# Performance work log

Hardware: AMD Instinct MI355X
Metric: run time of the kernel (lower is better)

The kernel has to match this reference:

```python
import jax, jax.numpy as jnp
import numpy as np

B, N, C = 4, 4096, 128

def setup_inputs() -> dict:
    key = jax.random.key(0)
    ks = jax.random.split(key, 7)
    s = 1.0 / np.sqrt(C)
    return {
        "x": jax.random.normal(ks[0], (B, N, C), dtype=jnp.float32),
        "Wq": jax.random.uniform(ks[1], (C, C), jnp.float32, -s, s),
        "bq": jax.random.uniform(ks[2], (C,), jnp.float32, -s, s),
        "Wk": jax.random.uniform(ks[3], (C, C), jnp.float32, -s, s),
        "bk": jax.random.uniform(ks[4], (C,), jnp.float32, -s, s),
        "Wv": jax.random.uniform(ks[5], (C, C), jnp.float32, -s, s),
        "bv": jax.random.uniform(ks[6], (C,), jnp.float32, -s, s),
    }

def reference(x, Wq, bq, Wk, bk, Wv, bv):
    # GELU-activated Q/K/V projections (torch default GELU = exact erf form)
    q = jax.nn.gelu(jnp.einsum("bnc,dc->bnd", x, Wq) + bq, approximate=False)
    k = jax.nn.gelu(jnp.einsum("bnc,dc->bnd", x, Wk) + bk, approximate=False)
    v = jax.nn.gelu(jnp.einsum("bnc,dc->bnd", x, Wv) + bv, approximate=False)
    # Unscaled attention: softmax(Q K^T) V
    scores = jnp.einsum("bnd,bmd->bnm", q, k)  # [B, N, N]
    attn = jax.nn.softmax(scores, axis=-1)
    return jnp.einsum("bnm,bmd->bnd", attn, v)
```

## Files before the change

### kernel.cpp

```cpp
#include <hip/hip_runtime.h>
#include <hip/hip_bf16.h>
#include <math.h>

#define BATCH 4
#define SEQ   4096
#define CDIM  128
#define NROWS (BATCH * SEQ)
#define KVB   32
#define NTILE (SEQ / KVB)
#define KTILE_B 8192
#define VTILE_B 8192
#define STAGE_B (KTILE_B + VTILE_B)
#define LOG2E 1.4426950408889634f

typedef __attribute__((ext_vector_type(4))) float    f32x4;
typedef __attribute__((ext_vector_type(8))) _Float16 half8;
typedef __attribute__((ext_vector_type(4))) short    bf16x4;
typedef __attribute__((ext_vector_type(8))) short    bf16x8;

__device__ __forceinline__ float bf2f(short s) {
  unsigned u = ((unsigned)(unsigned short)s) << 16;
  return __builtin_bit_cast(float, u);
}
__device__ __forceinline__ short f2bf(float f) {
  __hip_bfloat16 h = __float2bfloat16(f);
  return __builtin_bit_cast(short, h);
}
__device__ __forceinline__ float gelu_exact(float v) {
  return 0.5f * v * (1.0f + erff(v * 0.70710678118654752440f));
}
__device__ __forceinline__ float exp2_hw(float x) {
  float r;
  asm("v_exp_f32 %0, %1\n\ts_nop 0" : "=v"(r) : "v"(x));
  return r;
}
__device__ __forceinline__ int kswz_h(int r, int c) {
  int slot  = c >> 3;
  int slotp = (slot & 8) | ((slot ^ r) & 7);
  return r * 128 + slotp * 8 + (c & 7);
}
__device__ __forceinline__ void gl_lds16(const void* g, void* l) {
  __builtin_amdgcn_global_load_lds(
      (const __attribute__((address_space(1))) void*)g,
      (__attribute__((address_space(3))) void*)l, 16, 0, 0);
}

__global__ void wprep_kernel(const float* __restrict__ Wq,
                             const float* __restrict__ Wk,
                             const float* __restrict__ Wv,
                             _Float16* __restrict__ wfrag) {
  int mat = blockIdx.y;
  const float* W = (mat == 0) ? Wq : ((mat == 1) ? Wk : Wv);
  int i = blockIdx.x * 256 + threadIdx.x;
  int d = i >> 7, c = i & 127;
  int nt = d >> 4, qr = d & 15, cc = c >> 5, g = (c >> 3) & 3, j = c & 7;
  wfrag[(size_t)((((mat * 8 + nt) * 4 + cc) * 64) + 16 * g + qr) * 8 + j] =
      (_Float16)W[i];
}

__global__ __launch_bounds__(256) void proj_kernel(
    const float* __restrict__ x, const _Float16* __restrict__ wfrag,
    const float* __restrict__ bq, const float* __restrict__ bk,
    const float* __restrict__ bv,
    _Float16* __restrict__ qfrag, _Float16* __restrict__ kimg,
    short* __restrict__ vimg) {
  __shared__ __align__(16) char pls[16384];
  const int tid = threadIdx.x, wave = tid >> 6, lane = tid & 63;
  const int g = lane >> 4, qr = lane & 15;
  const int row0 = blockIdx.x * 64 + wave * 16;

  half8 xf[4];
#pragma unroll
  for (int c4 = 0; c4 < 4; ++c4) {
    const float* px = x + (size_t)(row0 + qr) * CDIM + 8 * g + 32 * c4;
    f32x4 a = *(const f32x4*)px;
    f32x4 bb = *(const f32x4*)(px + 4);
    half8 hx;
#pragma unroll
    for (int j = 0; j < 4; ++j) { hx[j] = (_Float16)a[j]; hx[4 + j] = (_Float16)bb[j]; }
    xf[c4] = hx;
  }

#pragma unroll
  for (int mat = 0; mat < 3; ++mat) {
    const float* bias = (mat == 0) ? bq : ((mat == 1) ? bk : bv);
    f32x4 acc[8];
#pragma unroll
    for (int nt = 0; nt < 8; ++nt) acc[nt] = (f32x4){0.f, 0.f, 0.f, 0.f};
#pragma unroll
    for (int nt = 0; nt < 8; ++nt)
#pragma unroll
      for (int c4 = 0; c4 < 4; ++c4) {
        half8 wf = *(const half8*)(wfrag +
            ((size_t)(((mat * 8 + nt) * 4 + c4) * 64) + lane) * 8);
        acc[nt] = __builtin_amdgcn_mfma_f32_16x16x32_f16(xf[c4], wf, acc[nt], 0, 0, 0);
      }

    short* ls = (short*)pls;
#pragma unroll
    for (int nt = 0; nt < 8; ++nt) {
      int col = 16 * nt + qr;
      float bi = bias[col];
#pragma unroll
      for (int r = 0; r < 4; ++r) {
        int rl = wave * 16 + 4 * g + r;
        float val = gelu_exact(acc[nt][r] + bi);
        int off;
        short sv;
        if (mat == 0) {
          int lane2 = ((col >> 3) & 3) * 16 + (rl & 15);
          off = ((wave * 4 + (col >> 5)) * 64 + lane2) * 8 + (col & 7);
          sv = __builtin_bit_cast(short, (_Float16)(val * LOG2E));
        } else if (mat == 1) {
          int tl = rl >> 5, rr = rl & 31;
          off = tl * 4096 + kswz_h(rr, col);
          sv = __builtin_bit_cast(short, (_Float16)val);
        } else {
          int tl = rl >> 5, rr = rl & 31;
          int klin = 8 * ((rr >> 2) & 3) + (rr & 3) + 4 * (rr >> 4);
          int slotp = (klin >> 3) ^ ((col >> 1) & 3);
          off = tl * 4096 + col * 32 + slotp * 8 + (klin & 7);
          sv = f2bf(val);
        }
        ls[off] = sv;
      }
    }
    __syncthreads();
    char* gdst = (mat == 0) ? (char*)qfrag + (size_t)blockIdx.x * 16384
               : (mat == 1) ? (char*)kimg + (size_t)blockIdx.x * 16384
                            : (char*)vimg + (size_t)blockIdx.x * 16384;
#pragma unroll
    for (int p = 0; p < 4; ++p)
      ((f32x4*)gdst)[tid + 256 * p] = ((const f32x4*)pls)[tid + 256 * p];
    __syncthreads();
  }
}

template <int NSPLIT>
__global__ __launch_bounds__(256, 2) void attn_kernel(
    const _Float16* __restrict__ qfrag, const char* __restrict__ kimg,
    const char* __restrict__ vimg, short* __restrict__ pacc,
    float* __restrict__ pml) {
  __shared__ __align__(16) char smem[2][STAGE_B];
  constexpr int NT = NTILE / NSPLIT;
  const int tid = threadIdx.x, wave = tid >> 6, lane = tid & 63;
  const int g = lane >> 4, qr = lane & 15;

  const int i = blockIdx.x;
  const int stream = i & (4 * NSPLIT - 1);
  const int b = stream / NSPLIT, sp = stream % NSPLIT;
  const int qg = i / (4 * NSPLIT);

  const int t0 = b * 256 + qg * 8 + wave * 2;
  half8 qf[2][4];
#pragma unroll
  for (int qs = 0; qs < 2; ++qs)
#pragma unroll
    for (int c4 = 0; c4 < 4; ++c4)
      qf[qs][c4] = *(const half8*)(qfrag +
          ((size_t)((t0 + qs) * 4 + c4) * 64 + lane) * 8);

  int koff[4];
#pragma unroll
  for (int c4 = 0; c4 < 4; ++c4) {
    int slot = 4 * c4 + g;
    int slotp = (slot & 8) | ((slot ^ qr) & 7);
    koff[c4] = qr * 256 + slotp * 16;
  }
  const int voff = qr * 64 + ((g ^ ((qr >> 1) & 3)) << 4);

  bf16x8 ones8;
#pragma unroll
  for (int j = 0; j < 8; ++j) ones8[j] = (short)0x3F80;

  const char* kp = kimg + ((size_t)b * NTILE + sp * NT) * KTILE_B + tid * 16;
  const char* vp = vimg + ((size_t)b * NTILE + sp * NT) * VTILE_B + tid * 16;

  auto stage = [&](char* buf) {
    gl_lds16(kp,        buf + tid * 16);
    gl_lds16(kp + 4096, buf + 4096 + tid * 16);
    gl_lds16(vp,        buf + 8192 + tid * 16);
    gl_lds16(vp + 4096, buf + 12288 + tid * 16);
    kp += KTILE_B;
    vp += VTILE_B;
  };

  f32x4 acc[2][8];
#pragma unroll
  for (int qs = 0; qs < 2; ++qs)
#pragma unroll
    for (int dt = 0; dt < 8; ++dt) acc[qs][dt] = (f32x4){0.f, 0.f, 0.f, 0.f};
  f32x4 lacc[2] = {(f32x4){0.f, 0.f, 0.f, 0.f}, (f32x4){0.f, 0.f, 0.f, 0.f}};
  float m[2] = {-INFINITY, -INFINITY};

  stage(smem[0]);

  auto phase = [&](const char* cur, char* other, bool do_stage) {
    asm volatile("s_waitcnt vmcnt(0) lgkmcnt(0)" ::: "memory");
    __builtin_amdgcn_s_barrier();
    if (do_stage) stage(other);

    f32x4 sA[2][2];
#pragma unroll
    for (int s = 0; s < 2; ++s) {
      half8 kf[4];
#pragma unroll
      for (int c4 = 0; c4 < 4; ++c4)
        kf[c4] = *(const half8*)(cur + koff[c4] + s * 4096);
      __builtin_amdgcn_s_setprio(1);
#pragma unroll
      for (int qs = 0; qs < 2; ++qs) {
        f32x4 tac = (f32x4){0.f, 0.f, 0.f, 0.f};
#pragma unroll
        for (int c4 = 0; c4 < 4; ++c4)
          tac = __builtin_amdgcn_mfma_f32_16x16x32_f16(kf[c4], qf[qs][c4], tac, 0, 0, 0);
        sA[qs][s] = tac;
      }
      __builtin_amdgcn_s_setprio(0);
    }

    bf16x8 pf8[2];
#pragma unroll
    for (int qs = 0; qs < 2; ++qs) {
      float tm = fmaxf(
          fmaxf(fmaxf(sA[qs][0][0], sA[qs][0][1]), fmaxf(sA[qs][0][2], sA[qs][0][3])),
          fmaxf(fmaxf(sA[qs][1][0], sA[qs][1][1]), fmaxf(sA[qs][1][2], sA[qs][1][3])));
      tm = fmaxf(tm, __shfl_xor(tm, 16, 64));
      tm = fmaxf(tm, __shfl_xor(tm, 32, 64));
      if (!__all(tm <= m[qs] + 8.0f)) {
        float mn = fmaxf(m[qs], tm);
        float alpha = exp2_hw(m[qs] - mn);
        m[qs] = mn;
        float af[4];
#pragma unroll
        for (int r = 0; r < 4; ++r) af[r] = __shfl(alpha, 4 * g + r, 64);
#pragma unroll
        for (int dt = 0; dt < 8; ++dt)
#pragma unroll
          for (int r = 0; r < 4; ++r) acc[qs][dt][r] *= af[r];
#pragma unroll
        for (int r = 0; r < 4; ++r) lacc[qs][r] *= af[r];
      }
#pragma unroll
      for (int e = 0; e < 8; ++e)
        pf8[qs][e] = f2bf(exp2_hw(sA[qs][e >> 2][e & 3] - m[qs]));
    }

    lacc[0] = __builtin_amdgcn_mfma_f32_16x16x32_bf16(pf8[0], ones8, lacc[0], 0, 0, 0);
    lacc[1] = __builtin_amdgcn_mfma_f32_16x16x32_bf16(pf8[1], ones8, lacc[1], 0, 0, 0);

#pragma unroll
    for (int dt = 0; dt < 8; ++dt) {
      bf16x8 v = *(const bf16x8*)(cur + KTILE_B + voff + dt * 1024);
      __builtin_amdgcn_s_setprio(1);
      acc[0][dt] = __builtin_amdgcn_mfma_f32_16x16x32_bf16(pf8[0], v, acc[0][dt], 0, 0, 0);
      acc[1][dt] = __builtin_amdgcn_mfma_f32_16x16x32_bf16(pf8[1], v, acc[1][dt], 0, 0, 0);
      __builtin_amdgcn_s_setprio(0);
    }
  };

#pragma unroll 1
  for (int it = 0; it < NT / 2; ++it) {
    phase(smem[0], smem[1], true);
    phase(smem[1], smem[0], it != NT / 2 - 1);
  }

  const int lrow0 = qg * 128 + wave * 32;
#pragma unroll
  for (int qs = 0; qs < 2; ++qs) {
#pragma unroll
    for (int dt = 0; dt < 8; ++dt)
#pragma unroll
      for (int r = 0; r < 4; ++r) {
        int grow = b * SEQ + lrow0 + qs * 16 + 4 * g + r;
        pacc[((size_t)sp * NROWS + grow) * CDIM + 16 * dt + qr] =
            f2bf(acc[qs][dt][r]);
      }
    if (g == 0) {
      int grow = b * SEQ + lrow0 + qs * 16 + qr;
      pml[((size_t)sp * NROWS + grow) * 2 + 0] = m[qs];
    }
    if (qr == 0) {
#pragma unroll
      for (int r = 0; r < 4; ++r) {
        int grow = b * SEQ + lrow0 + qs * 16 + 4 * g + r;
        pml[((size_t)sp * NROWS + grow) * 2 + 1] = lacc[qs][r];
      }
    }
  }
}

template <int NSPLIT>
__global__ __launch_bounds__(256) void combine_kernel(
    const short* __restrict__ pacc, const float* __restrict__ pml,
    float* __restrict__ out) {
  int idx = blockIdx.x * 256 + threadIdx.x;
  int row = idx >> 4, c8 = idx & 15;
  float mm[NSPLIT], ll[NSPLIT];
  float M = -INFINITY;
#pragma unroll
  for (int h = 0; h < NSPLIT; ++h) {
    mm[h] = pml[((size_t)h * NROWS + row) * 2 + 0];
    ll[h] = pml[((size_t)h * NROWS + row) * 2 + 1];
    M = fmaxf(M, mm[h]);
  }
  float o[8];
#pragma unroll
  for (int j = 0; j < 8; ++j) o[j] = 0.f;
  float wl = 0.f;
#pragma unroll
  for (int h = 0; h < NSPLIT; ++h) {
    float w = exp2f(mm[h] - M);
    wl += w * ll[h];
    bf16x8 a = ((const bf16x8*)pacc)[((size_t)h * NROWS + row) * 16 + c8];
#pragma unroll
    for (int j = 0; j < 8; ++j) o[j] += w * bf2f(a[j]);
  }
  float inv = 1.0f / wl;
  f32x4 o0 = {o[0] * inv, o[1] * inv, o[2] * inv, o[3] * inv};
  f32x4 o1 = {o[4] * inv, o[5] * inv, o[6] * inv, o[7] * inv};
  ((f32x4*)out)[(size_t)row * 32 + c8 * 2 + 0] = o0;
  ((f32x4*)out)[(size_t)row * 32 + c8 * 2 + 1] = o1;
}

extern "C" void kernel_launch(void* const* d_in, const int* in_sizes, int n_in,
                              void* d_out, int out_size, void* d_ws, size_t ws_size,
                              hipStream_t stream) {
  const float* x  = (const float*)d_in[0];
  const float* Wq = (const float*)d_in[1];
  const float* bq = (const float*)d_in[2];
  const float* Wk = (const float*)d_in[3];
  const float* bk = (const float*)d_in[4];
  const float* Wv = (const float*)d_in[5];
  const float* bv = (const float*)d_in[6];
  float* out = (float*)d_out;

  char* ws = (char*)d_ws;
  _Float16* qfrag = (_Float16*)(ws);
  char*     kimg  = ws + (4u << 20);
  char*     vimg  = ws + (8u << 20);
  _Float16* wfrag = (_Float16*)(ws + (12u << 20));
  char*     tail  = ws + (12u << 20) + (256u << 10);

  const size_t need8 = (12u << 20) + (256u << 10) +
                       (size_t)8 * NROWS * 8 + (size_t)8 * NROWS * CDIM * 2;

  wprep_kernel<<<dim3(64, 3), 256, 0, stream>>>(Wq, Wk, Wv, wfrag);
  proj_kernel<<<NROWS / 64, 256, 0, stream>>>(x, wfrag, bq, bk, bv,
                                              qfrag, (_Float16*)kimg, (short*)vimg);
  if (ws_size >= need8) {
    float* pml  = (float*)tail;
    short* pacc = (short*)(tail + (size_t)8 * NROWS * 8);
    attn_kernel<8><<<1024, 256, 0, stream>>>(qfrag, kimg, vimg, pacc, pml);
    combine_kernel<8><<<NROWS * 16 / 256, 256, 0, stream>>>(pacc, pml, out);
  } else {
    float* pml  = (float*)tail;
    short* pacc = (short*)(tail + (size_t)4 * NROWS * 8);
    attn_kernel<4><<<512, 256, 0, stream>>>(qfrag, kimg, vimg, pacc, pml);
    combine_kernel<4><<<NROWS * 16 / 256, 256, 0, stream>>>(pacc, pml, out);
  }
}
```

Before: 147.1 us.

## Split K and V staging into a triple-buffered K, double-buffered V pipeline

```diff
diff --git a/kernel.cpp b/kernel.cpp
--- a/kernel.cpp
+++ b/kernel.cpp
@@ -10,7 +10,6 @@
 #define NTILE (SEQ / KVB)
 #define KTILE_B 8192
 #define VTILE_B 8192
-#define STAGE_B (KTILE_B + VTILE_B)
 #define LOG2E 1.4426950408889634f
 
 typedef __attribute__((ext_vector_type(4))) float    f32x4;
@@ -136,15 +135,35 @@
   }
 }
 
+#define PHASE(KB, VB, KW, VW, IK, IV, VMK, VMV)                         \
+  do {                                                                  \
+    if (IK) stageK(KW);                                                 \
+    asm volatile("s_waitcnt vmcnt(" VMK ")" ::: "memory");              \
+    __builtin_amdgcn_s_barrier();                                       \
+    if (IV) stageV(VW);                                                 \
+    qk_sm(KB);                                                          \
+    asm volatile("s_waitcnt vmcnt(" VMV ")" ::: "memory");              \
+    __builtin_amdgcn_s_barrier();                                       \
+    pv(VB);                                                             \
+  } while (0)
+
 template <int NSPLIT>
 __global__ __launch_bounds__(256, 2) void attn_kernel(
     const _Float16* __restrict__ qfrag, const char* __restrict__ kimg,
     const char* __restrict__ vimg, short* __restrict__ pacc,
     float* __restrict__ pml) {
-  __shared__ __align__(16) char smem[2][STAGE_B];
+  __shared__ __align__(16) char smem[3 * KTILE_B + 2 * VTILE_B];
   constexpr int NT = NTILE / NSPLIT;
+  static_assert((NT - 4) % 6 == 0, "steady loop needs (NT-4) % 6 == 0");
+  constexpr int NSTEADY = (NT - 4) / 6;
   const int tid = threadIdx.x, wave = tid >> 6, lane = tid & 63;
   const int g = lane >> 4, qr = lane & 15;
+
+  char* const kbuf0 = smem;
+  char* const kbuf1 = smem + KTILE_B;
+  char* const kbuf2 = smem + 2 * KTILE_B;
+  char* const vbuf0 = smem + 3 * KTILE_B;
+  char* const vbuf1 = smem + 3 * KTILE_B + VTILE_B;
 
   const int i = blockIdx.x;
   const int stream = i & (4 * NSPLIT - 1);
@@ -176,12 +195,14 @@
   const char* kp = kimg + ((size_t)b * NTILE + sp * NT) * KTILE_B + tid * 16;
   const char* vp = vimg + ((size_t)b * NTILE + sp * NT) * VTILE_B + tid * 16;
 
-  auto stage = [&](char* buf) {
+  auto stageK = [&](char* buf) {
     gl_lds16(kp,        buf + tid * 16);
     gl_lds16(kp + 4096, buf + 4096 + tid * 16);
-    gl_lds16(vp,        buf + 8192 + tid * 16);
-    gl_lds16(vp + 4096, buf + 12288 + tid * 16);
     kp += KTILE_B;
+  };
+  auto stageV = [&](char* buf) {
+    gl_lds16(vp,        buf + tid * 16);
+    gl_lds16(vp + 4096, buf + 4096 + tid * 16);
     vp += VTILE_B;
   };
 
@@ -192,21 +213,16 @@
     for (int dt = 0; dt < 8; ++dt) acc[qs][dt] = (f32x4){0.f, 0.f, 0.f, 0.f};
   f32x4 lacc[2] = {(f32x4){0.f, 0.f, 0.f, 0.f}, (f32x4){0.f, 0.f, 0.f, 0.f}};
   float m[2] = {-INFINITY, -INFINITY};
-
-  stage(smem[0]);
-
-  auto phase = [&](const char* cur, char* other, bool do_stage) {
-    asm volatile("s_waitcnt vmcnt(0) lgkmcnt(0)" ::: "memory");
-    __builtin_amdgcn_s_barrier();
-    if (do_stage) stage(other);
-
+  bf16x8 pf8[2];
+
+  auto qk_sm = [&](const char* kb) {
     f32x4 sA[2][2];
 #pragma unroll
     for (int s = 0; s < 2; ++s) {
       half8 kf[4];
 #pragma unroll
       for (int c4 = 0; c4 < 4; ++c4)
-        kf[c4] = *(const half8*)(cur + koff[c4] + s * 4096);
+        kf[c4] = *(const half8*)(kb + koff[c4] + s * 4096);
       __builtin_amdgcn_s_setprio(1);
 #pragma unroll
       for (int qs = 0; qs < 2; ++qs) {
@@ -218,8 +234,6 @@
       }
       __builtin_amdgcn_s_setprio(0);
     }
-
-    bf16x8 pf8[2];
 #pragma unroll
     for (int qs = 0; qs < 2; ++qs) {
       float tm = fmaxf(
@@ -245,13 +259,14 @@
       for (int e = 0; e < 8; ++e)
         pf8[qs][e] = f2bf(exp2_hw(sA[qs][e >> 2][e & 3] - m[qs]));
     }
-
     lacc[0] = __builtin_amdgcn_mfma_f32_16x16x32_bf16(pf8[0], ones8, lacc[0], 0, 0, 0);
     lacc[1] = __builtin_amdgcn_mfma_f32_16x16x32_bf16(pf8[1], ones8, lacc[1], 0, 0, 0);
-
+  };
+
+  auto pv = [&](const char* vb) {
 #pragma unroll
     for (int dt = 0; dt < 8; ++dt) {
-      bf16x8 v = *(const bf16x8*)(cur + KTILE_B + voff + dt * 1024);
+      bf16x8 v = *(const bf16x8*)(vb + voff + dt * 1024);
       __builtin_amdgcn_s_setprio(1);
       acc[0][dt] = __builtin_amdgcn_mfma_f32_16x16x32_bf16(pf8[0], v, acc[0][dt], 0, 0, 0);
       acc[1][dt] = __builtin_amdgcn_mfma_f32_16x16x32_bf16(pf8[1], v, acc[1][dt], 0, 0, 0);
@@ -259,11 +274,21 @@
     }
   };
 
+  stageK(kbuf0); stageV(vbuf0); stageK(kbuf1);
+
+  PHASE(kbuf0, vbuf0, kbuf2, vbuf1, true,  true,  "6", "6");
+  PHASE(kbuf1, vbuf1, kbuf0, vbuf0, true,  true,  "6", "4");
 #pragma unroll 1
-  for (int it = 0; it < NT / 2; ++it) {
-    phase(smem[0], smem[1], true);
-    phase(smem[1], smem[0], it != NT / 2 - 1);
-  }
+  for (int it = 0; it < NSTEADY; ++it) {
+    PHASE(kbuf2, vbuf0, kbuf1, vbuf1, true, true, "6", "4");
+    PHASE(kbuf0, vbuf1, kbuf2, vbuf0, true, true, "6", "4");
+    PHASE(kbuf1, vbuf0, kbuf0, vbuf1, true, true, "6", "4");
+    PHASE(kbuf2, vbuf1, kbuf1, vbuf0, true, true, "6", "4");
+    PHASE(kbuf0, vbuf0, kbuf2, vbuf1, true, true, "6", "4");
+    PHASE(kbuf1, vbuf1, kbuf0, vbuf0, true, true, "6", "4");
+  }
+  PHASE(kbuf2, vbuf0, kbuf0, vbuf1, false, true,  "4", "2");
+  PHASE(kbuf0, vbuf1, kbuf0, vbuf0, false, false, "2", "0");
 
   const int lrow0 = qg * 128 + wave * 32;
 #pragma unroll
@@ -355,8 +380,8 @@
     combine_kernel<8><<<NROWS * 16 / 256, 256, 0, stream>>>(pacc, pml, out);
   } else {
     float* pml  = (float*)tail;
-    short* pacc = (short*)(tail + (size_t)4 * NROWS * 8);
-    attn_kernel<4><<<512, 256, 0, stream>>>(qfrag, kimg, vimg, pacc, pml);
-    combine_kernel<4><<<NROWS * 16 / 256, 256, 0, stream>>>(pacc, pml, out);
-  }
-}
+    short* pacc = (short*)(tail + (size_t)2 * NROWS * 8);
+    attn_kernel<2><<<256, 256, 0, stream>>>(qfrag, kimg, vimg, pacc, pml);
+    combine_kernel<2><<<NROWS * 16 / 256, 256, 0, stream>>>(pacc, pml, out);
+  }
+}
```

After: 148.8 us. About the same (+1.2%).
